# Performance work log

Hardware: AMD Instinct MI355X
Metric: run time of the kernel (lower is better)

## Reference

```python
import jax, jax.numpy as jnp
import numpy as np

B, C, N, M_MODES, EMB = 8, 64, 2048, 32, 256
MFREQ = 2 * M_MODES * (2 * M_MODES - 1)  # 4032
SCALE = 1.0 / (C * C)


def setup_inputs() -> dict:
    key = jax.random.key(0)
    ks = jax.random.split(key, 16)
    d = {
        "x": jax.random.normal(ks[0], (B, C, N), jnp.float32),
        "emb": jax.random.normal(ks[1], (B, EMB), jnp.float32),
        "Vf_re": jax.random.normal(ks[2], (MFREQ, N), jnp.float32),
        "Vf_im": jax.random.normal(ks[3], (MFREQ, N), jnp.float32),
        "Vi_re": jax.random.normal(ks[4], (N, MFREQ), jnp.float32),
        "Vi_im": jax.random.normal(ks[5], (N, MFREQ), jnp.float32),
        "w1_re": SCALE * jax.random.uniform(ks[6], (C, C, M_MODES, M_MODES), jnp.float32),
        "w1_im": SCALE * jax.random.uniform(ks[7], (C, C, M_MODES, M_MODES), jnp.float32),
        "w2_re": SCALE * jax.random.uniform(ks[8], (C, C, M_MODES, M_MODES), jnp.float32),
        "w2_im": SCALE * jax.random.uniform(ks[9], (C, C, M_MODES, M_MODES), jnp.float32),
        "m1_re": SCALE * jax.random.uniform(ks[10], (1, M_MODES, M_MODES, EMB), jnp.float32),
        "m1_im": SCALE * jax.random.uniform(ks[11], (1, M_MODES, M_MODES, EMB), jnp.float32),
        "m2_re": SCALE * jax.random.uniform(ks[12], (1, M_MODES, M_MODES, EMB), jnp.float32),
        "m2_im": SCALE * jax.random.uniform(ks[13], (1, M_MODES, M_MODES, EMB), jnp.float32),
    }
    return d


def _spectral_conv(x, emb, Vf, Vi, w1, w2, mod1, mod2):
    m = M_MODES
    # nuft.forward: [B,N,C] complex -> [B,MFREQ,C]
    xc = jnp.transpose(x, (0, 2, 1)).astype(jnp.complex64)
    x_nfft = jnp.einsum('mn,bnc->bmc', Vf, xc)
    # [B,C,2m,2m-1]
    x_ft = jnp.transpose(x_nfft, (0, 2, 1)).reshape(x.shape[0], C, 2 * m, 2 * m - 1)
    embc = emb.astype(jnp.complex64)[:, None, None, :]  # [B,1,1,EMB]
    phi1 = jnp.sum(mod1 * embc, axis=-1)  # [B,m,m]
    phi2 = jnp.sum(mod2 * embc, axis=-1)
    out1 = jnp.einsum('bixy,ioxy->boxy', x_ft[:, :, :m, :m], w1)
    out2 = jnp.einsum('bixy,ioxy->boxy', x_ft[:, :, -m:, :m], w2)
    mod1b = phi1[:, None, :, :] * out1
    mod2b = phi2[:, None, :, :] * out2
    out_ft = jnp.concatenate([mod1b, mod2b], axis=2)  # [B,C,2m,m]
    xf = out_ft.reshape(x.shape[0], C, 2 * m * m)
    # Hermitian-symmetry reconstruction: flip over mode AND channel dims, conj
    xf2 = jnp.conj(jnp.flip(xf[..., 2 * m:], axis=(-2, -1)))
    xf = jnp.concatenate([xf, xf2], axis=-1)  # [B,C,MFREQ]
    xf = jnp.transpose(xf, (0, 2, 1))  # [B,MFREQ,C]
    out = jnp.einsum('nm,bmc->bnc', Vi, xf)  # nuft.inverse -> [B,N,C]
    out = jnp.transpose(out, (0, 2, 1)) / N * 2
    return out.real


def reference(x, emb, Vf_re, Vf_im, Vi_re, Vi_im, w1_re, w1_im, w2_re, w2_im, m1_re, m1_im, m2_re, m2_im):
    Vf = Vf_re + 1j * Vf_im
    Vi = Vi_re + 1j * Vi_im
    w1 = w1_re + 1j * w1_im
    w2 = w2_re + 1j * w2_im
    mod1 = m1_re + 1j * m1_im
    mod2 = m2_re + 1j * m2_im
    return _spectral_conv(x, emb, Vf, Vi, w1, w2, mod1, mod2)
```

## Files before the change

kernel.cpp:

```cpp
#include <hip/hip_runtime.h>

#define BB    8
#define CC    64
#define NN    2048
#define GG    2048
#define MFREQ 4032

typedef __attribute__((ext_vector_type(4))) float f32x4;
typedef __attribute__((ext_vector_type(8))) short bf16x8;

static __device__ __forceinline__ unsigned short f2bf(float f) {
    union { float f; unsigned u; } v; v.f = f;
    unsigned r = v.u + 0x7fff + ((v.u >> 16) & 1);
    return (unsigned short)(r >> 16);
}

static __device__ __forceinline__ unsigned int pk2(float lo, float hi) {
    return (unsigned int)f2bf(lo) | ((unsigned int)f2bf(hi) << 16);
}

static __device__ __forceinline__ uint4 pack_unit(float4 a, float4 b, int mode) {
    uint4 o;
    if (mode == 3) { o.x = o.y = o.z = o.w = 0u; return o; }
    if (mode == 2) {
        o.x = pk2(a.w, a.z); o.y = pk2(a.y, a.x);
        o.z = pk2(b.w, b.z); o.w = pk2(b.y, b.x);
    } else if (mode == 1) {
        o.x = pk2(-a.x, -a.y); o.y = pk2(-a.z, -a.w);
        o.z = pk2(-b.x, -b.y); o.w = pk2(-b.z, -b.w);
    } else {
        o.x = pk2(a.x, a.y); o.y = pk2(a.z, a.w);
        o.z = pk2(b.x, b.y); o.w = pk2(b.z, b.w);
    }
    return o;
}

#define ASYNC_COPY16(gp, lp)                                                        \
    __builtin_amdgcn_global_load_lds(                                               \
        (const __attribute__((address_space(1))) unsigned int*)(gp),                \
        (__attribute__((address_space(3))) unsigned int*)(lp), 16, 0, 0)

static __device__ __forceinline__ void decode_unit(int uid,
        const float* __restrict__ vf_re, const float* __restrict__ vf_im,
        const float* __restrict__ x,
        const float* __restrict__ vi_re, const float* __restrict__ vi_im,
        unsigned short* __restrict__ af, unsigned short* __restrict__ xb,
        unsigned short* __restrict__ mi,
        const float*& pa, const float*& pb, unsigned short*& dst, int& mode) {
    if (uid < 1048576) {
        int m = uid >> 8;
        int q8 = (uid & 255) * 8;
        int g = m & 2047;
        int f = (g >> 5) * 63 + (g & 31);
        const float* src = (m < 2048 ? vf_re : vf_im) + (size_t)f * 2048 + q8;
        pa = src; pb = src + 4; dst = af + (size_t)m * 2048 + q8; mode = 0;
    } else if (uid < 1179648) {
        int v = uid - 1048576;
        int q8 = v * 8;
        pa = x + q8; pb = x + q8 + 4; dst = xb + q8; mode = 0;
    } else {
        int v = uid - 1179648;
        int n = v >> 10;
        int q8 = (v & 1023) * 8;
        int region = q8 >> 11;
        int off = q8 & 2047;
        dst = mi + (size_t)n * 8192 + q8;
        if (region == 0) {
            pa = vi_re + (size_t)n * MFREQ + off; pb = pa + 4; mode = 0;
        } else if (region == 1) {
            pa = vi_im + (size_t)n * MFREQ + off; pb = pa + 4; mode = 1;
        } else {
            const float* src = (region == 2 ? vi_re : vi_im) + (size_t)n * MFREQ;
            if (off < 64) { pa = src; pb = src; mode = 3; }
            else { pa = src + 4092 - off; pb = src + 4088 - off; mode = 2; }
        }
    }
}

__global__ __launch_bounds__(256) void prep_all(const float* __restrict__ vf_re,
                                                const float* __restrict__ vf_im,
                                                const float* __restrict__ x,
                                                const float* __restrict__ vi_re,
                                                const float* __restrict__ vi_im,
                                                const float* __restrict__ m1_re,
                                                const float* __restrict__ m1_im,
                                                const float* __restrict__ m2_re,
                                                const float* __restrict__ m2_im,
                                                const float* __restrict__ emb,
                                                unsigned short* __restrict__ af,
                                                unsigned short* __restrict__ xb,
                                                unsigned short* __restrict__ mi,
                                                float* __restrict__ phi_re,
                                                float* __restrict__ phi_im) {
    __shared__ float sr4[4], si4[4];
    int blk = blockIdx.x;
    int t = threadIdx.x;

    if (blk < 1280) {
        const int STRIDE = 1280 * 256;
        int uid0 = blk * 256 + t;
        const float *pa0, *pb0; unsigned short* d0; int md0;
        decode_unit(uid0, vf_re, vf_im, x, vi_re, vi_im, af, xb, mi, pa0, pb0, d0, md0);
        float4 A0 = *(const float4*)pa0;
        float4 B0 = *(const float4*)pb0;
        #pragma unroll
        for (int i = 1; i <= 10; ++i) {
            const float *pa1 = pa0, *pb1 = pb0; unsigned short* d1 = d0; int md1 = md0;
            float4 A1 = A0, B1 = B0;
            if (i < 10) {
                decode_unit(uid0 + i * STRIDE, vf_re, vf_im, x, vi_re, vi_im,
                            af, xb, mi, pa1, pb1, d1, md1);
                A1 = *(const float4*)pa1;
                B1 = *(const float4*)pb1;
            }
            uint4 o = pack_unit(A0, B0, md0);
            *(uint4*)d0 = o;
            A0 = A1; B0 = B1; d0 = d1; md0 = md1;
            pa0 = pa1; pb0 = pb1;
        }
    } else {
        int g = blk - 1280, e = t;
        int xy = g & 1023;
        const float* mr = (g < 1024 ? m1_re : m2_re) + xy * 256;
        const float* mp = (g < 1024 ? m1_im : m2_im) + xy * 256;
        float vr = mr[e], vi = mp[e];
        for (int bb = 0; bb < 8; ++bb) {
            float em = emb[bb * 256 + e];
            float pr = vr * em, pi = vi * em;
            for (int s = 32; s > 0; s >>= 1) { pr += __shfl_down(pr, s); pi += __shfl_down(pi, s); }
            int wid = e >> 6;
            if ((e & 63) == 0) { sr4[wid] = pr; si4[wid] = pi; }
            __syncthreads();
            if (e == 0) {
                phi_re[bb * 2048 + g] = sr4[0] + sr4[1] + sr4[2] + sr4[3];
                phi_im[bb * 2048 + g] = si4[0] + si4[1] + si4[2] + si4[3];
            }
            __syncthreads();
        }
    }
}

template<int TM>
__global__ __launch_bounds__(256, 2) void gemm_sk(const unsigned short* __restrict__ A,
                                                  const unsigned short* __restrict__ Bm,
                                                  float* __restrict__ P,
                                                  int M, int N, int K, int Kper, int ilv) {
    constexpr int FI = TM / 32;
    __shared__ unsigned short As[TM * 64];
    __shared__ unsigned short Bs[TM * 64];
    int t = threadIdx.x;
    int lane = t & 63, w = t >> 6;
    int m0 = blockIdx.y * TM, n0 = blockIdx.x * TM;
    int z = blockIdx.z;
    int kbase = z * Kper;
    int wm = (w >> 1) * (TM / 2), wn = (w & 1) * (TM / 2);
    int lr = lane & 15, quad = lane >> 4;
    int rsub = lane >> 3, slot = lane & 7;

    f32x4 acc[FI][FI] = {};

    for (int kk = kbase; kk < kbase + Kper; kk += 64) {
        __syncthreads();
        #pragma unroll
        for (int l = 0; l < FI; ++l) {
            int r = (w * FI + l) * 8 + rsub;
            int c = slot ^ (r & 7);
            ASYNC_COPY16(A + (size_t)(m0 + r) * K + kk + c * 8, As + r * 64 + slot * 8);
            ASYNC_COPY16(Bm + (size_t)(n0 + r) * K + kk + c * 8, Bs + r * 64 + slot * 8);
        }
        __syncthreads();
        #pragma unroll
        for (int ks = 0; ks < 2; ++ks) {
            bf16x8 af[FI], bfr[FI];
            #pragma unroll
            for (int i = 0; i < FI; ++i) {
                int row = wm + i * 16 + lr;
                int q = (ks * 4 + quad) ^ (row & 7);
                af[i] = *(const bf16x8*)(As + row * 64 + q * 8);
                int rowb = wn + i * 16 + lr;
                int qb = (ks * 4 + quad) ^ (rowb & 7);
                bfr[i] = *(const bf16x8*)(Bs + rowb * 64 + qb * 8);
            }
            #pragma unroll
            for (int i = 0; i < FI; ++i)
            #pragma unroll
            for (int j = 0; j < FI; ++j)
                acc[i][j] = __builtin_amdgcn_mfma_f32_16x16x32_bf16(af[i], bfr[j], acc[i][j], 0, 0, 0);
        }
    }
    float* Pz = P + (size_t)z * M * N;
    size_t rstride = ilv ? 2 : (size_t)N;
    #pragma unroll
    for (int i = 0; i < FI; ++i)
    #pragma unroll
    for (int j = 0; j < FI; ++j) {
        int rr = m0 + wm + i * 16 + quad * 4;
        int cc = n0 + wn + j * 16 + lr;
        size_t base = ilv ? ((size_t)cc * 4096 + (size_t)(rr & 2047) * 2 + (rr >> 11))
                          : ((size_t)rr * N + cc);
        float* cp = Pz + base;
        f32x4 v = acc[i][j];
        cp[0]           = v.x;
        cp[rstride]     = v.y;
        cp[2 * rstride] = v.z;
        cp[3 * rstride] = v.w;
    }
}

__global__ __launch_bounds__(256) void reduce_k(const float* __restrict__ P,
                                                float* __restrict__ out,
                                                int S, size_t elems, float alpha) {
    size_t idx = ((size_t)blockIdx.x * 256 + threadIdx.x) * 4;
    float4 s = *(const float4*)(P + idx);
    for (int zz = 1; zz < S; ++zz) {
        float4 v = *(const float4*)(P + (size_t)zz * elems + idx);
        s.x += v.x; s.y += v.y; s.z += v.z; s.w += v.w;
    }
    s.x *= alpha; s.y *= alpha; s.z *= alpha; s.w *= alpha;
    *(float4*)(out + idx) = s;
}

__global__ __launch_bounds__(256) void middle_k2(const float* __restrict__ O1,
                                                 const float* __restrict__ w1_re,
                                                 const float* __restrict__ w1_im,
                                                 const float* __restrict__ w2_re,
                                                 const float* __restrict__ w2_im,
                                                 const float* __restrict__ phi_re,
                                                 const float* __restrict__ phi_im,
                                                 unsigned short* __restrict__ Yt) {
    __shared__ float sO1[128 * 64];
    int t = threadIdx.x;
    int bx = blockIdx.x;
    int g0 = (bx & 63) * 32;
    int o0 = ((bx >> 6) & 1) * 32;
    int b0 = (bx >> 7) * 2;
    const float* wre = (g0 < 1024 ? w1_re : w2_re);
    const float* wim = (g0 < 1024 ? w1_im : w2_im);
    int xyb = g0 & 1023;

    #pragma unroll
    for (int s = 0; s < 8; ++s) {
        int idx = s * 256 + t;
        int row = idx >> 4;
        int off = (idx & 15) * 4;
        ASYNC_COPY16(O1 + (size_t)(b0 * 64 + row) * 4096 + g0 * 2 + off,
                     sO1 + row * 64 + off);
    }
    __syncthreads();

    int ol = t >> 3, gq = t & 7;
    int o = o0 + ol;
    float accr[2][4] = {}, acci[2][4] = {};

    #pragma unroll 4
    for (int i = 0; i < 64; ++i) {
        size_t wrow = (size_t)(i * 64 + o) * 1024 + xyb + gq * 4;
        float4 wr = *(const float4*)(wre + wrow);
        float4 wi = *(const float4*)(wim + wrow);
        #pragma unroll
        for (int b = 0; b < 2; ++b) {
            const float* op = sO1 + (b * 64 + i) * 64 + gq * 8;
            float4 oa = *(const float4*)op;
            float4 ob = *(const float4*)(op + 4);
            accr[b][0] += wr.x * oa.x - wi.x * oa.y;
            acci[b][0] += wr.x * oa.y + wi.x * oa.x;
            accr[b][1] += wr.y * oa.z - wi.y * oa.w;
            acci[b][1] += wr.y * oa.w + wi.y * oa.z;
            accr[b][2] += wr.z * ob.x - wi.z * ob.y;
            acci[b][2] += wr.z * ob.y + wi.z * ob.x;
            accr[b][3] += wr.w * ob.z - wi.w * ob.w;
            acci[b][3] += wr.w * ob.w + wi.w * ob.z;
        }
    }

    int g4 = g0 + gq * 4;
    #pragma unroll
    for (int b = 0; b < 2; ++b) {
        int bb = b0 + b;
        float4 pr = *(const float4*)(phi_re + bb * 2048 + g4);
        float4 pi = *(const float4*)(phi_im + bb * 2048 + g4);
        ushort4 vre, vim;
        vre.x = f2bf(pr.x * accr[b][0] - pi.x * acci[b][0]);
        vim.x = f2bf(pr.x * acci[b][0] + pi.x * accr[b][0]);
        vre.y = f2bf(pr.y * accr[b][1] - pi.y * acci[b][1]);
        vim.y = f2bf(pr.y * acci[b][1] + pi.y * accr[b][1]);
        vre.z = f2bf(pr.z * accr[b][2] - pi.z * acci[b][2]);
        vim.z = f2bf(pr.z * acci[b][2] + pi.z * accr[b][2]);
        vre.w = f2bf(pr.w * accr[b][3] - pi.w * acci[b][3]);
        vim.w = f2bf(pr.w * acci[b][3] + pi.w * accr[b][3]);
        size_t r0 = (size_t)(bb * 64 + o) * 8192;
        size_t rf = (size_t)(bb * 64 + 63 - o) * 8192;
        *(ushort4*)(Yt + r0 + g4)        = vre;
        *(ushort4*)(Yt + r0 + 2048 + g4) = vim;
        *(ushort4*)(Yt + rf + 4096 + g4) = vre;
        *(ushort4*)(Yt + rf + 6144 + g4) = vim;
    }
}

extern "C" void kernel_launch(void* const* d_in, const int* in_sizes, int n_in,
                              void* d_out, int out_size, void* d_ws, size_t ws_size,
                              hipStream_t stream) {
    const float* x     = (const float*)d_in[0];
    const float* emb   = (const float*)d_in[1];
    const float* vf_re = (const float*)d_in[2];
    const float* vf_im = (const float*)d_in[3];
    const float* vi_re = (const float*)d_in[4];
    const float* vi_im = (const float*)d_in[5];
    const float* w1_re = (const float*)d_in[6];
    const float* w1_im = (const float*)d_in[7];
    const float* w2_re = (const float*)d_in[8];
    const float* w2_im = (const float*)d_in[9];
    const float* m1_re = (const float*)d_in[10];
    const float* m1_im = (const float*)d_in[11];
    const float* m2_re = (const float*)d_in[12];
    const float* m2_im = (const float*)d_in[13];

    char* ws = (char*)d_ws;
    unsigned short* Af = (unsigned short*)(ws);
    unsigned short* Xb = (unsigned short*)(ws + 16777216);
    unsigned short* Mi = (unsigned short*)(ws + 18874368);
    float*          O1 = (float*)(ws + 85983232);
    float*       PhiRe = (float*)(ws + 94371840);
    float*       PhiIm = (float*)(ws + 94437376);
    unsigned short* Yt = (unsigned short*)(ws + 94502912);
    float*          P  = (float*)(ws + 102891520);
    float* out = (float*)d_out;

    prep_all<<<3328, 256, 0, stream>>>(vf_re, vf_im, x, vi_re, vi_im,
                                       m1_re, m1_im, m2_re, m2_im, emb,
                                       Af, Xb, Mi, PhiRe, PhiIm);

    gemm_sk<64><<<dim3(8, 64, 1), 256, 0, stream>>>(Af, Xb, O1, 4096, 512, 2048, 2048, 1);

    middle_k2<<<512, 256, 0, stream>>>(O1, w1_re, w1_im, w2_re, w2_im,
                                       PhiRe, PhiIm, Yt);

    gemm_sk<128><<<dim3(16, 4, 8), 256, 0, stream>>>(Yt, Mi, P, 512, 2048, 8192, 1024, 0);
    reduce_k<<<1024, 256, 0, stream>>>(P, out, 8, (size_t)512 * 2048, 1.0f / 1024.0f);
}
```

Baseline: 314.0 us.

## Double-buffer LDS tiles in split-K GEMM to overlap loads with MFMA

The bf16 GEMM now keeps two LDS buffers for the A and B tiles and issues the async copies for the next K tile before computing on the current one. A partial vmcnt wait plus a raw s_barrier replaces the two __syncthreads per iteration, so global-to-LDS latency can overlap the matrix-core work. This doubles LDS use, which may lower occupancy under launch_bounds(256,2). It also depends on the vmcnt count matching the number of copies issued per stage.

Result: no change. 315.9 us (+0.6%).

```diff
diff --git a/kernel.cpp b/kernel.cpp
--- a/kernel.cpp
+++ b/kernel.cpp
@@ -146,8 +146,8 @@
                                                   float* __restrict__ P,
                                                   int M, int N, int K, int Kper, int ilv) {
     constexpr int FI = TM / 32;
-    __shared__ unsigned short As[TM * 64];
-    __shared__ unsigned short Bs[TM * 64];
+    __shared__ unsigned short As[2][TM * 64];
+    __shared__ unsigned short Bs[2][TM * 64];
     int t = threadIdx.x;
     int lane = t & 63, w = t >> 6;
     int m0 = blockIdx.y * TM, n0 = blockIdx.x * TM;
@@ -159,16 +159,28 @@
 
     f32x4 acc[FI][FI] = {};
 
-    for (int kk = kbase; kk < kbase + Kper; kk += 64) {
-        __syncthreads();
+    auto stage = [&](int kk, int buf) {
         #pragma unroll
         for (int l = 0; l < FI; ++l) {
             int r = (w * FI + l) * 8 + rsub;
             int c = slot ^ (r & 7);
-            ASYNC_COPY16(A + (size_t)(m0 + r) * K + kk + c * 8, As + r * 64 + slot * 8);
-            ASYNC_COPY16(Bm + (size_t)(n0 + r) * K + kk + c * 8, Bs + r * 64 + slot * 8);
-        }
-        __syncthreads();
+            ASYNC_COPY16(A + (size_t)(m0 + r) * K + kk + c * 8, &As[buf][r * 64 + slot * 8]);
+            ASYNC_COPY16(Bm + (size_t)(n0 + r) * K + kk + c * 8, &Bs[buf][r * 64 + slot * 8]);
+        }
+    };
+
+    int nt = Kper >> 6;
+    stage(kbase, 0);
+    int cur = 0;
+    for (int tt = 0; tt < nt; ++tt) {
+        if (tt + 1 < nt) {
+            stage(kbase + (tt + 1) * 64, cur ^ 1);
+            __builtin_amdgcn_sched_barrier(0);
+            asm volatile("s_waitcnt vmcnt(%0)" :: "n"(2 * FI) : "memory");
+        } else {
+            asm volatile("s_waitcnt vmcnt(0)" ::: "memory");
+        }
+        asm volatile("s_barrier" ::: "memory");
         #pragma unroll
         for (int ks = 0; ks < 2; ++ks) {
             bf16x8 af[FI], bfr[FI];
@@ -176,10 +188,10 @@
             for (int i = 0; i < FI; ++i) {
                 int row = wm + i * 16 + lr;
                 int q = (ks * 4 + quad) ^ (row & 7);
-                af[i] = *(const bf16x8*)(As + row * 64 + q * 8);
+                af[i] = *(const bf16x8*)(&As[cur][row * 64 + q * 8]);
                 int rowb = wn + i * 16 + lr;
                 int qb = (ks * 4 + quad) ^ (rowb & 7);
-                bfr[i] = *(const bf16x8*)(Bs + rowb * 64 + qb * 8);
+                bfr[i] = *(const bf16x8*)(&Bs[cur][rowb * 64 + qb * 8]);
             }
             #pragma unroll
             for (int i = 0; i < FI; ++i)
@@ -187,7 +199,10 @@
             for (int j = 0; j < FI; ++j)
                 acc[i][j] = __builtin_amdgcn_mfma_f32_16x16x32_bf16(af[i], bfr[j], acc[i][j], 0, 0, 0);
         }
-    }
+        asm volatile("s_barrier" ::: "memory");
+        cur ^= 1;
+    }
+
     float* Pz = P + (size_t)z * M * N;
     size_t rstride = ilv ? 2 : (size_t)N;
     #pragma unroll
```
